# Optimization experiments

Measured on AMD Instinct MI355X. Metric: run time of the kernel, lower is better.

The kernel has to match this reference:

```python
import jax, jax.numpy as jnp
import numpy as np

N_GRID = 16       # n
CELL_SIDE = 2.0
LATENT = 16       # latent_dim (pooling_dim for type_='social')
HIDDEN = 128
OUT_DIM = 128
CONSTANT = 0.0
NUM_TRACKS = 1024


def setup_inputs() -> dict:
    key = jax.random.key(0)
    ks = jax.random.split(key, 6)
    T = NUM_TRACKS
    hidden_state = jax.random.normal(ks[0], (T, HIDDEN), jnp.float32)
    # positions spread over a ~20m scene; obs2 is obs1 plus a small step (velocity)
    obs1 = jax.random.uniform(ks[1], (T, 2), jnp.float32) * 20.0
    obs2 = obs1 + jax.random.normal(ks[2], (T, 2), jnp.float32) * 0.5
    W_enc = jax.random.normal(ks[3], (HIDDEN, LATENT), jnp.float32) / np.sqrt(HIDDEN)
    b_enc = jnp.zeros((LATENT,), jnp.float32)
    in_dim = N_GRID * N_GRID * LATENT  # 4096
    W_emb = jax.random.normal(ks[4], (in_dim, OUT_DIM), jnp.float32) / np.sqrt(in_dim)
    b_emb = jnp.zeros((OUT_DIM,), jnp.float32)
    return dict(hidden_state=hidden_state, obs1=obs1, obs2=obs2,
                W_enc=W_enc, b_enc=b_enc, W_emb=W_emb, b_emb=b_emb)


def _social_grid(hidden_state, obs2, W_enc, b_enc):
    T = obs2.shape[0]
    # NaN rows -> 0 (mask = isnan(obs).any(dim=1))
    obs = jnp.where(jnp.isnan(obs2).any(axis=1, keepdims=True), 0.0, obs2)
    # static off-diagonal neighbor indices: row i lists all j != i  [T, T-1]
    cols = np.broadcast_to(np.arange(T), (T, T))
    nbr = cols[~np.eye(T, dtype=bool)].reshape(T, T - 1)
    rel = obs[nbr] - obs[:, None, :]                 # [T, T-1, 2] obs[j]-obs[i]
    vals = hidden_state[nbr] @ W_enc + b_enc         # [T, T-1, LATENT]
    # grid cell coordinates (pool_size=1, front=False)
    oij = rel / CELL_SIDE + N_GRID / 2.0             # [T, T-1, 2]
    in_range = jnp.sum((oij < 0) | (oij >= N_GRID), axis=2) == 0  # [T, T-1]
    oij_i = jnp.where(in_range[..., None], oij, 0.0).astype(jnp.int32)
    vals = jnp.where(in_range[..., None], vals, CONSTANT)
    oi = oij_i[..., 0] * N_GRID + oij_i[..., 1]      # flat cell index [T, T-1]
    occ = jnp.full((T, N_GRID * N_GRID, LATENT), CONSTANT, vals.dtype)
    occ = occ.at[jnp.arange(T)[:, None], oi].set(vals)
    # [T, LATENT, n, n]; blur_size=1 and lp_pool with kernel=pool_size=1 are identity
    return jnp.transpose(occ, (0, 2, 1)).reshape(T, LATENT, N_GRID, N_GRID)


def reference(hidden_state, obs1, obs2, W_enc, b_enc, W_emb, b_emb):
    grid = _social_grid(hidden_state, obs2, W_enc, b_enc)
    T = grid.shape[0]
    flat = grid.reshape(T, -1)                       # [T, n*n*LATENT]
    return jax.nn.relu(flat @ W_emb + b_emb)         # [T, OUT_DIM]
```

## Files before the change

### kernel.cpp

```cpp
#include <hip/hip_runtime.h>
#include <hip/hip_bf16.h>
#include <math.h>

#define T_TRACKS 1024
#define HIDDEN 128
#define LATENT 16
#define NGRID 16
#define NCELLS 256
#define KDIM 4096
#define OUTD 128

typedef unsigned short ushort_t;
typedef __attribute__((ext_vector_type(8))) short frag_ab;
typedef __attribute__((ext_vector_type(4))) float f32x4;

static __device__ inline ushort_t f2bf(float x) {
    __hip_bfloat16 h = __float2bfloat16(x);
    return *reinterpret_cast<ushort_t*>(&h);
}

#define WS_VALS 0
#define WS_WT   32768
#define WS_OCC  1081344
#define WS_PART 9469952
#define WS_NEED (9469952 + 8388608)

__global__ __launch_bounds__(256) void prep_kernel(const float* __restrict__ hidden,
                                                   const float* __restrict__ W_enc,
                                                   const float* __restrict__ b_enc,
                                                   const float* __restrict__ W_emb,
                                                   ushort_t* __restrict__ vals_bf16,
                                                   ushort_t* __restrict__ W_t) {
    const int b = blockIdx.x;
    const int tid = threadIdx.x;
    if (b < 64) {
        int idx = b * 256 + tid;
        int j = idx >> 4, l = idx & 15;
        const float* h = hidden + j * HIDDEN;
        float acc = b_enc[l];
#pragma unroll 8
        for (int k = 0; k < HIDDEN; k++) acc += h[k] * W_enc[k * LATENT + l];
        vals_bf16[idx] = f2bf(acc);
    } else {
        int idx = (b - 64) * 256 + tid;
        int kc = idx >> 7;
        int o = idx & 127;
        ushort_t tmp[8];
#pragma unroll
        for (int u = 0; u < 8; u++) tmp[u] = f2bf(W_emb[(kc * 8 + u) * OUTD + o]);
        *reinterpret_cast<uint4*>(W_t + o * KDIM + kc * 8) = *reinterpret_cast<uint4*>(tmp);
    }
}

__global__ __launch_bounds__(256) void occ_kernel(const float* __restrict__ obs2,
                                                  const ushort_t* __restrict__ vals_bf16,
                                                  ushort_t* __restrict__ occ) {
    const int i = blockIdx.x;
    const int tid = threadIdx.x;
    __shared__ int owner[NCELLS];
    __shared__ ushort_t socc[LATENT * NCELLS];
    owner[tid] = -1;

    float oix = obs2[i * 2 + 0];
    float oiy = obs2[i * 2 + 1];
    if (isnan(oix) || isnan(oiy)) { oix = 0.0f; oiy = 0.0f; }
    __syncthreads();

    for (int j = tid; j < T_TRACKS; j += 256) {
        if (j == i) continue;
        float ox = obs2[j * 2 + 0];
        float oy = obs2[j * 2 + 1];
        if (isnan(ox) || isnan(oy)) { ox = 0.0f; oy = 0.0f; }
        float gx = (ox - oix) * 0.5f + 8.0f;
        float gy = (oy - oiy) * 0.5f + 8.0f;
        bool inr = (gx >= 0.0f) && (gx < 16.0f) && (gy >= 0.0f) && (gy < 16.0f);
        int c = inr ? ((int)gx * NGRID + (int)gy) : 0;
        atomicMax(&owner[c], j);
    }
    __syncthreads();

    {
        const int c = tid;
        int j = owner[c];
        bool valid = (j >= 0);
        if (c == 0 && valid) {
            float ox = obs2[j * 2 + 0];
            float oy = obs2[j * 2 + 1];
            if (isnan(ox) || isnan(oy)) { ox = 0.0f; oy = 0.0f; }
            float gx = (ox - oix) * 0.5f + 8.0f;
            float gy = (oy - oiy) * 0.5f + 8.0f;
            valid = (gx >= 0.0f) && (gx < 16.0f) && (gy >= 0.0f) && (gy < 16.0f);
        }
        int jj = (j >= 0) ? j : 0;
        ushort_t vv[16];
        *reinterpret_cast<uint4*>(vv)     = *reinterpret_cast<const uint4*>(vals_bf16 + jj * LATENT);
        *reinterpret_cast<uint4*>(vv + 8) = *reinterpret_cast<const uint4*>(vals_bf16 + jj * LATENT + 8);
#pragma unroll
        for (int l = 0; l < LATENT; l++) {
            socc[l * NCELLS + c] = valid ? vv[l] : (ushort_t)0;
        }
    }
    __syncthreads();

    uint4* dst = reinterpret_cast<uint4*>(occ + i * KDIM);
    const uint4* src = reinterpret_cast<const uint4*>(socc);
    dst[tid]       = src[tid];
    dst[tid + 256] = src[tid + 256];
}

#define BK 128
#define LDSTR 136
__global__ __launch_bounds__(256) void gemm_kernel(const ushort_t* __restrict__ occ,
                                                   const ushort_t* __restrict__ W_t,
                                                   float* __restrict__ partial) {
    const int tid = threadIdx.x;
    const int kt = blockIdx.x & 15;
    const int mt = blockIdx.x >> 4;
    const int wave = tid >> 6;
    const int lane = tid & 63;
    const int lrow = lane & 15;
    const int quad = lane >> 4;

    __shared__ ushort_t As[64 * LDSTR];
    __shared__ ushort_t Bs[128 * LDSTR];

    f32x4 acc[8];
#pragma unroll
    for (int nt = 0; nt < 8; nt++) acc[nt] = (f32x4){0.f, 0.f, 0.f, 0.f};

    for (int chunk = 0; chunk < 2; chunk++) {
        const int k0 = kt * 256 + chunk * BK;
        for (int g = tid; g < 1024; g += 256) {
            int r = g >> 4, cs = g & 15;
            uint4 v = *reinterpret_cast<const uint4*>(occ + (mt * 64 + r) * KDIM + k0 + cs * 8);
            *reinterpret_cast<uint4*>(As + r * LDSTR + cs * 8) = v;
        }
        for (int g = tid; g < 2048; g += 256) {
            int n = g >> 4, cs = g & 15;
            uint4 v = *reinterpret_cast<const uint4*>(W_t + n * KDIM + k0 + cs * 8);
            *reinterpret_cast<uint4*>(Bs + n * LDSTR + cs * 8) = v;
        }
        __syncthreads();
#pragma unroll
        for (int ks = 0; ks < 4; ks++) {
            const int koff = ks * 32 + quad * 8;
            frag_ab a = *reinterpret_cast<const frag_ab*>(&As[(wave * 16 + lrow) * LDSTR + koff]);
#pragma unroll
            for (int nt = 0; nt < 8; nt++) {
                frag_ab bfr = *reinterpret_cast<const frag_ab*>(&Bs[(nt * 16 + lrow) * LDSTR + koff]);
                acc[nt] = __builtin_amdgcn_mfma_f32_16x16x32_bf16(a, bfr, acc[nt], 0, 0, 0);
            }
        }
        __syncthreads();
    }
    float* pt = partial + (size_t)kt * (T_TRACKS * OUTD) + (mt * 64) * OUTD;
#pragma unroll
    for (int nt = 0; nt < 8; nt++) {
        int n = nt * 16 + lrow;
#pragma unroll
        for (int reg = 0; reg < 4; reg++) {
            int m = wave * 16 + quad * 4 + reg;
            pt[m * OUTD + n] = acc[nt][reg];
        }
    }
}

__global__ __launch_bounds__(256) void reduce_kernel(const float* __restrict__ partial,
                                                     const float* __restrict__ b_emb,
                                                     float* __restrict__ out) {
    int idx = blockIdx.x * 256 + threadIdx.x;
    const float4* p4 = reinterpret_cast<const float4*>(partial);
    float4 s = p4[idx];
#pragma unroll
    for (int kt = 1; kt < 16; kt++) {
        float4 v = p4[kt * 32768 + idx];
        s.x += v.x; s.y += v.y; s.z += v.z; s.w += v.w;
    }
    float4 bv = reinterpret_cast<const float4*>(b_emb)[idx & 31];
    float4 r;
    r.x = fmaxf(s.x + bv.x, 0.0f);
    r.y = fmaxf(s.y + bv.y, 0.0f);
    r.z = fmaxf(s.z + bv.z, 0.0f);
    r.w = fmaxf(s.w + bv.w, 0.0f);
    reinterpret_cast<float4*>(out)[idx] = r;
}

__global__ __launch_bounds__(256) void vals_kernel_f32(const float* __restrict__ hidden,
                                                       const float* __restrict__ W_enc,
                                                       const float* __restrict__ b_enc,
                                                       float* __restrict__ vals) {
    int idx = blockIdx.x * 256 + threadIdx.x;
    int j = idx >> 4, l = idx & 15;
    const float* h = hidden + j * HIDDEN;
    float acc = b_enc[l];
#pragma unroll 8
    for (int k = 0; k < HIDDEN; k++) acc += h[k] * W_enc[k * LATENT + l];
    vals[idx] = acc;
}

__global__ __launch_bounds__(256) void pool_kernel_f32(const float* __restrict__ obs2,
                                                       const float* __restrict__ vals,
                                                       const float* __restrict__ W_emb,
                                                       const float* __restrict__ b_emb,
                                                       float* __restrict__ out) {
    const int i = blockIdx.x;
    const int tid = threadIdx.x;
    __shared__ int owner[NCELLS];
    __shared__ float occ[NCELLS * LATENT];
    __shared__ float partial[OUTD];
    owner[tid] = -1;
    float oix = obs2[i * 2 + 0];
    float oiy = obs2[i * 2 + 1];
    if (isnan(oix) || isnan(oiy)) { oix = 0.0f; oiy = 0.0f; }
    __syncthreads();
    for (int j = tid; j < T_TRACKS; j += 256) {
        if (j == i) continue;
        float ox = obs2[j * 2 + 0], oy = obs2[j * 2 + 1];
        if (isnan(ox) || isnan(oy)) { ox = 0.0f; oy = 0.0f; }
        float gx = (ox - oix) * 0.5f + 8.0f;
        float gy = (oy - oiy) * 0.5f + 8.0f;
        bool inr = (gx >= 0.0f) && (gx < 16.0f) && (gy >= 0.0f) && (gy < 16.0f);
        int c = inr ? ((int)gx * NGRID + (int)gy) : 0;
        atomicMax(&owner[c], j);
    }
    __syncthreads();
    {
        int j = owner[tid];
        bool valid = false;
        if (j >= 0) {
            float ox = obs2[j * 2 + 0], oy = obs2[j * 2 + 1];
            if (isnan(ox) || isnan(oy)) { ox = 0.0f; oy = 0.0f; }
            float gx = (ox - oix) * 0.5f + 8.0f;
            float gy = (oy - oiy) * 0.5f + 8.0f;
            valid = (gx >= 0.0f) && (gx < 16.0f) && (gy >= 0.0f) && (gy < 16.0f);
        }
        const float* vj = vals + (j >= 0 ? j : 0) * LATENT;
#pragma unroll
        for (int l = 0; l < LATENT; l++) occ[tid * LATENT + l] = valid ? vj[l] : 0.0f;
    }
    __syncthreads();
    const int o = tid & (OUTD - 1);
    const int half = tid >> 7;
    const int cbase = half * 128;
    float acc = 0.0f;
    for (int c = cbase; c < cbase + 128; c++) {
#pragma unroll
        for (int l = 0; l < LATENT; l++)
            acc += occ[c * LATENT + l] * W_emb[(l * NCELLS + c) * OUTD + o];
    }
    if (half == 0) partial[o] = acc;
    __syncthreads();
    if (half == 1) out[i * OUTD + o] = fmaxf(acc + partial[o] + b_emb[o], 0.0f);
}

extern "C" void kernel_launch(void* const* d_in, const int* in_sizes, int n_in,
                              void* d_out, int out_size, void* d_ws, size_t ws_size,
                              hipStream_t stream) {
    const float* hidden = (const float*)d_in[0];
    const float* obs2   = (const float*)d_in[2];
    const float* W_enc  = (const float*)d_in[3];
    const float* b_enc  = (const float*)d_in[4];
    const float* W_emb  = (const float*)d_in[5];
    const float* b_emb  = (const float*)d_in[6];
    float* out = (float*)d_out;

    if (ws_size < (size_t)WS_NEED) {
        float* vals = (float*)d_ws;
        vals_kernel_f32<<<(T_TRACKS * LATENT) / 256, 256, 0, stream>>>(hidden, W_enc, b_enc, vals);
        pool_kernel_f32<<<T_TRACKS, 256, 0, stream>>>(obs2, vals, W_emb, b_emb, out);
        return;
    }

    char* ws = (char*)d_ws;
    ushort_t* vals_bf16 = (ushort_t*)(ws + WS_VALS);
    ushort_t* W_t       = (ushort_t*)(ws + WS_WT);
    ushort_t* occ       = (ushort_t*)(ws + WS_OCC);
    float*    partial   = (float*)(ws + WS_PART);

    prep_kernel<<<320, 256, 0, stream>>>(hidden, W_enc, b_enc, W_emb, vals_bf16, W_t);
    occ_kernel<<<T_TRACKS, 256, 0, stream>>>(obs2, vals_bf16, occ);
    gemm_kernel<<<256, 256, 0, stream>>>(occ, W_t, partial);
    reduce_kernel<<<128, 256, 0, stream>>>(partial, b_emb, out);
}
```

Measured before the change: 90.90 us.

## Replace dense occupancy tensor with per-cell owner map gathered in GEMM

Removes the separate occupancy kernel and its 8 MB bf16 occ buffer. Instead, prep_kernel computes a compact 16-bit owner index per (track, cell), 16 tracks per block, and stores the latent values transposed. The GEMM builds its A tile on the fly by gathering vals_t through those owner indices, with each K-tile mapped to one latent channel. This cuts one launch and most of the global traffic for A, at the cost of scalar gathers during the A-tile load.

```diff
diff --git a/kernel.cpp b/kernel.cpp
--- a/kernel.cpp
+++ b/kernel.cpp
@@ -20,16 +20,18 @@
 }
 
 #define WS_VALS 0
-#define WS_WT   32768
-#define WS_OCC  1081344
-#define WS_PART 9469952
-#define WS_NEED (9469952 + 8388608)
+#define WS_OWN  32768
+#define WS_WT   557056
+#define WS_PART 1605632
+#define WS_NEED (1605632 + 8388608)
 
 __global__ __launch_bounds__(256) void prep_kernel(const float* __restrict__ hidden,
+                                                   const float* __restrict__ obs2,
                                                    const float* __restrict__ W_enc,
                                                    const float* __restrict__ b_enc,
                                                    const float* __restrict__ W_emb,
-                                                   ushort_t* __restrict__ vals_bf16,
+                                                   ushort_t* __restrict__ vals_t,
+                                                   ushort_t* __restrict__ owner,
                                                    ushort_t* __restrict__ W_t) {
     const int b = blockIdx.x;
     const int tid = threadIdx.x;
@@ -40,8 +42,8 @@
         float acc = b_enc[l];
 #pragma unroll 8
         for (int k = 0; k < HIDDEN; k++) acc += h[k] * W_enc[k * LATENT + l];
-        vals_bf16[idx] = f2bf(acc);
-    } else {
+        vals_t[l * T_TRACKS + j] = f2bf(acc);
+    } else if (b < 320) {
         int idx = (b - 64) * 256 + tid;
         int kc = idx >> 7;
         int o = idx & 127;
@@ -49,73 +51,55 @@
 #pragma unroll
         for (int u = 0; u < 8; u++) tmp[u] = f2bf(W_emb[(kc * 8 + u) * OUTD + o]);
         *reinterpret_cast<uint4*>(W_t + o * KDIM + kc * 8) = *reinterpret_cast<uint4*>(tmp);
-    }
-}
-
-__global__ __launch_bounds__(256) void occ_kernel(const float* __restrict__ obs2,
-                                                  const ushort_t* __restrict__ vals_bf16,
-                                                  ushort_t* __restrict__ occ) {
-    const int i = blockIdx.x;
-    const int tid = threadIdx.x;
-    __shared__ int owner[NCELLS];
-    __shared__ ushort_t socc[LATENT * NCELLS];
-    owner[tid] = -1;
-
-    float oix = obs2[i * 2 + 0];
-    float oiy = obs2[i * 2 + 1];
-    if (isnan(oix) || isnan(oiy)) { oix = 0.0f; oiy = 0.0f; }
-    __syncthreads();
-
-    for (int j = tid; j < T_TRACKS; j += 256) {
-        if (j == i) continue;
-        float ox = obs2[j * 2 + 0];
-        float oy = obs2[j * 2 + 1];
-        if (isnan(ox) || isnan(oy)) { ox = 0.0f; oy = 0.0f; }
-        float gx = (ox - oix) * 0.5f + 8.0f;
-        float gy = (oy - oiy) * 0.5f + 8.0f;
-        bool inr = (gx >= 0.0f) && (gx < 16.0f) && (gy >= 0.0f) && (gy < 16.0f);
-        int c = inr ? ((int)gx * NGRID + (int)gy) : 0;
-        atomicMax(&owner[c], j);
-    }
-    __syncthreads();
-
-    {
-        const int c = tid;
-        int j = owner[c];
-        bool valid = (j >= 0);
-        if (c == 0 && valid) {
-            float ox = obs2[j * 2 + 0];
-            float oy = obs2[j * 2 + 1];
-            if (isnan(ox) || isnan(oy)) { ox = 0.0f; oy = 0.0f; }
-            float gx = (ox - oix) * 0.5f + 8.0f;
-            float gy = (oy - oiy) * 0.5f + 8.0f;
-            valid = (gx >= 0.0f) && (gx < 16.0f) && (gy >= 0.0f) && (gy < 16.0f);
-        }
-        int jj = (j >= 0) ? j : 0;
-        ushort_t vv[16];
-        *reinterpret_cast<uint4*>(vv)     = *reinterpret_cast<const uint4*>(vals_bf16 + jj * LATENT);
-        *reinterpret_cast<uint4*>(vv + 8) = *reinterpret_cast<const uint4*>(vals_bf16 + jj * LATENT + 8);
-#pragma unroll
-        for (int l = 0; l < LATENT; l++) {
-            socc[l * NCELLS + c] = valid ? vv[l] : (ushort_t)0;
-        }
-    }
-    __syncthreads();
-
-    uint4* dst = reinterpret_cast<uint4*>(occ + i * KDIM);
-    const uint4* src = reinterpret_cast<const uint4*>(socc);
-    dst[tid]       = src[tid];
-    dst[tid + 256] = src[tid + 256];
+    } else {
+        __shared__ float2 sobs[T_TRACKS];
+        __shared__ int own[16][NCELLS];
+        const int rbase = (b - 320) * 16;
+        for (int q = tid; q < T_TRACKS; q += 256) {
+            float2 o = reinterpret_cast<const float2*>(obs2)[q];
+            if (isnan(o.x) || isnan(o.y)) { o.x = 0.0f; o.y = 0.0f; }
+            sobs[q] = o;
+        }
+        for (int q = tid; q < 16 * NCELLS; q += 256) (&own[0][0])[q] = -1;
+        __syncthreads();
+        {
+            const int r = tid & 15;
+            const int i = rbase + r;
+            const float oix = sobs[i].x, oiy = sobs[i].y;
+            for (int j = tid >> 4; j < T_TRACKS; j += 16) {
+                if (j == i) continue;
+                float gx = (sobs[j].x - oix) * 0.5f + 8.0f;
+                float gy = (sobs[j].y - oiy) * 0.5f + 8.0f;
+                bool inr = (gx >= 0.0f) && (gx < 16.0f) && (gy >= 0.0f) && (gy < 16.0f);
+                int c = inr ? ((int)gx * NGRID + (int)gy) : 0;
+                atomicMax(&own[r][c], j);
+            }
+        }
+        __syncthreads();
+        for (int q = tid; q < 16 * NCELLS; q += 256) {
+            int rr = q >> 8, c = q & 255;
+            int j = own[rr][c];
+            bool valid = (j >= 0);
+            if (valid && c == 0) {
+                float oix = sobs[rbase + rr].x, oiy = sobs[rbase + rr].y;
+                float gx = (sobs[j].x - oix) * 0.5f + 8.0f;
+                float gy = (sobs[j].y - oiy) * 0.5f + 8.0f;
+                valid = (gx >= 0.0f) && (gx < 16.0f) && (gy >= 0.0f) && (gy < 16.0f);
+            }
+            owner[(rbase + rr) * NCELLS + c] = valid ? (ushort_t)(j + 1) : (ushort_t)0;
+        }
+    }
 }
 
 #define BK 128
 #define LDSTR 136
-__global__ __launch_bounds__(256) void gemm_kernel(const ushort_t* __restrict__ occ,
+__global__ __launch_bounds__(256) void gemm_kernel(const ushort_t* __restrict__ owner,
+                                                   const ushort_t* __restrict__ vals_t,
                                                    const ushort_t* __restrict__ W_t,
                                                    float* __restrict__ partial) {
     const int tid = threadIdx.x;
-    const int kt = blockIdx.x & 15;
-    const int mt = blockIdx.x >> 4;
+    const int kt = blockIdx.x >> 4;
+    const int mt = blockIdx.x & 15;
     const int wave = tid >> 6;
     const int lane = tid & 63;
     const int lrow = lane & 15;
@@ -124,20 +108,27 @@
     __shared__ ushort_t As[64 * LDSTR];
     __shared__ ushort_t Bs[128 * LDSTR];
 
+    const ushort_t* vrow = vals_t + kt * T_TRACKS;
+
     f32x4 acc[8];
 #pragma unroll
     for (int nt = 0; nt < 8; nt++) acc[nt] = (f32x4){0.f, 0.f, 0.f, 0.f};
 
     for (int chunk = 0; chunk < 2; chunk++) {
-        const int k0 = kt * 256 + chunk * BK;
-        for (int g = tid; g < 1024; g += 256) {
-            int r = g >> 4, cs = g & 15;
-            uint4 v = *reinterpret_cast<const uint4*>(occ + (mt * 64 + r) * KDIM + k0 + cs * 8);
-            *reinterpret_cast<uint4*>(As + r * LDSTR + cs * 8) = v;
+        const int c0 = chunk * BK;
+        for (int q = tid; q < 2048; q += 256) {
+            int r = q >> 5, c4 = (q & 31) * 4;
+            ushort4 o4 = *reinterpret_cast<const ushort4*>(owner + (mt * 64 + r) * NCELLS + c0 + c4);
+            ushort4 v;
+            v.x = o4.x ? vrow[o4.x - 1] : (ushort_t)0;
+            v.y = o4.y ? vrow[o4.y - 1] : (ushort_t)0;
+            v.z = o4.z ? vrow[o4.z - 1] : (ushort_t)0;
+            v.w = o4.w ? vrow[o4.w - 1] : (ushort_t)0;
+            *reinterpret_cast<ushort4*>(As + r * LDSTR + c4) = v;
         }
         for (int g = tid; g < 2048; g += 256) {
             int n = g >> 4, cs = g & 15;
-            uint4 v = *reinterpret_cast<const uint4*>(W_t + n * KDIM + k0 + cs * 8);
+            uint4 v = *reinterpret_cast<const uint4*>(W_t + n * KDIM + kt * 256 + c0 + cs * 8);
             *reinterpret_cast<uint4*>(Bs + n * LDSTR + cs * 8) = v;
         }
         __syncthreads();
@@ -272,13 +263,12 @@
     }
 
     char* ws = (char*)d_ws;
-    ushort_t* vals_bf16 = (ushort_t*)(ws + WS_VALS);
-    ushort_t* W_t       = (ushort_t*)(ws + WS_WT);
-    ushort_t* occ       = (ushort_t*)(ws + WS_OCC);
-    float*    partial   = (float*)(ws + WS_PART);
-
-    prep_kernel<<<320, 256, 0, stream>>>(hidden, W_enc, b_enc, W_emb, vals_bf16, W_t);
-    occ_kernel<<<T_TRACKS, 256, 0, stream>>>(obs2, vals_bf16, occ);
-    gemm_kernel<<<256, 256, 0, stream>>>(occ, W_t, partial);
+    ushort_t* vals_t = (ushort_t*)(ws + WS_VALS);
+    ushort_t* owner  = (ushort_t*)(ws + WS_OWN);
+    ushort_t* W_t    = (ushort_t*)(ws + WS_WT);
+    float*    partial = (float*)(ws + WS_PART);
+
+    prep_kernel<<<384, 256, 0, stream>>>(hidden, obs2, W_enc, b_enc, W_emb, vals_t, owner, W_t);
+    gemm_kernel<<<256, 256, 0, stream>>>(owner, vals_t, W_t, partial);
     reduce_kernel<<<128, 256, 0, stream>>>(partial, b_emb, out);
 }
```

New measurement: 96.53 us. 1.06x slower.
